# Kernel tuning notes

Hardware: AMD Instinct MI355X
Metric: run time of the kernel (lower is better)

The kernel has to match this reference:

```python
import jax, jax.numpy as jnp
import numpy as np

TEMP = 0.02          # init kwarg temp (sim is multiplied by temp before exp)
OTHERWEIGHT = 0.5    # init kwarg otherweight (cross-half weighting)


def _labels(overlap_inds, bs):
    # labels1: class i for group i of feats1; labels2: same class if overlap,
    # else a fresh class starting at K, incrementing per non-overlap group.
    K = overlap_inds.shape[0]
    labels1 = jnp.repeat(jnp.arange(K), bs)
    non = (overlap_inds == 0).astype(jnp.int32)
    excl = jnp.cumsum(non) - non  # exclusive prefix count of non-overlap groups
    cls2 = jnp.where(overlap_inds.astype(bool), jnp.arange(K), K + excl)
    labels2 = jnp.repeat(cls2, bs)
    return jnp.concatenate([labels1, labels2])


def setup_inputs() -> dict:
    key = jax.random.key(0)
    k1, k2, k3 = jax.random.split(key, 3)
    K, BS, F = 8, 256, 512
    feats1 = jax.random.normal(k1, (K * BS, F), dtype=jnp.float32)
    feats2 = jax.random.normal(k2, (K * BS, F), dtype=jnp.float32)
    overlap_inds = jax.random.randint(k3, (K,), 0, 2).astype(jnp.int32)
    return {"feats1": feats1, "feats2": feats2, "overlap_inds": overlap_inds, "bs": BS}


def reference(feats1, feats2, overlap_inds, bs):
    n1 = feats1.shape[0]
    feats = jnp.concatenate([feats1, feats2])         # [N, F]
    n = feats.shape[0]
    labels = _labels(overlap_inds, bs)                # [N]

    same = labels[None, :] == labels[:, None]         # [N, N] bool
    sim = jnp.exp((feats @ feats.T) * TEMP)           # [N, N]

    eye = jnp.eye(n, dtype=bool)
    pos_mask = same & ~eye
    neg_mask = ~same

    # cross_weighting: OTHERWEIGHT on cross-half blocks, 1.0 within each half
    half = jnp.arange(n) < n1
    cross = jnp.where(half[:, None] == half[None, :], 1.0, OTHERWEIGHT)

    # per-row negative sum; loss = sum over positives of cw * -log(pos/neg_sum)
    neg_sum = jnp.sum(jnp.where(neg_mask, sim, 0.0), axis=1)        # [N]
    loss_terms = jnp.where(pos_mask, cross * -jnp.log(sim / neg_sum[:, None]), 0.0)
    total_pos = jnp.sum(pos_mask).astype(jnp.float32)
    loss = loss_terms.sum() / total_pos

    # accuracy: a positive counts iff it beats every negative in its row
    # (mean(0)==1.0 over strict > comparisons <=> pos > max(neg))
    max_neg = jnp.max(jnp.where(neg_mask, sim, -jnp.inf), axis=1)   # [N]
    correct = jnp.where(pos_mask, (sim > max_neg[:, None]).astype(jnp.float32), 0.0)
    acc = correct.sum() / total_pos
    return acc, loss
```

## Files before the change

kernel.cpp:

```cpp
#include <hip/hip_runtime.h>


#define KGRP 8
#define FD   512
#define N1T  2048
#define NT   4096
#define TEMPW 0.02f

typedef __attribute__((ext_vector_type(8))) short short8;
typedef __attribute__((ext_vector_type(4))) float f32x4;
typedef unsigned short ushort_t;


__device__ __forceinline__ unsigned enc_ord(float f) {
  unsigned u = __float_as_uint(f);
  return (u & 0x80000000u) ? ~u : (u | 0x80000000u);
}
__device__ __forceinline__ float dec_ord(unsigned u) {
  unsigned b = (u & 0x80000000u) ? (u & 0x7fffffffu) : ~u;
  return __uint_as_float(b);
}

__device__ __forceinline__ ushort_t f2bf(float f) {
  unsigned u = __float_as_uint(f);
  u = (u + 0x7fffu + ((u >> 16) & 1u)) >> 16;
  return (ushort_t)u;
}

__device__ __forceinline__ void gld16(const void* g, void* l) {
  __builtin_amdgcn_global_load_lds(
      (const __attribute__((address_space(1))) unsigned*)g,
      (__attribute__((address_space(3))) unsigned*)l, 16, 0, 0);
}

__global__ __launch_bounds__(256) void prep_k(
    const float* __restrict__ f1, const float* __restrict__ f2,
    ushort_t* __restrict__ bf,
    float* __restrict__ neg_sum, unsigned* __restrict__ neg_max,
    float* __restrict__ sumS, float* __restrict__ corr,
    int* __restrict__ cnts, int* __restrict__ neg_list,
    int* __restrict__ pos_list, const int* __restrict__ ov)
{
  const int b = blockIdx.x, t = threadIdx.x;

  {
    int i = b * 256 + t;
    size_t base = (size_t)i * 8;
    const size_t half = (size_t)N1T * FD;
    const float* sp = (base < half) ? (f1 + base) : (f2 + (base - half));
    float4 u0 = ((const float4*)sp)[0];
    float4 u1 = ((const float4*)sp)[1];
    short8 o;
    o[0] = (short)f2bf(u0.x); o[1] = (short)f2bf(u0.y);
    o[2] = (short)f2bf(u0.z); o[3] = (short)f2bf(u0.w);
    o[4] = (short)f2bf(u1.x); o[5] = (short)f2bf(u1.y);
    o[6] = (short)f2bf(u1.z); o[7] = (short)f2bf(u1.w);
    *(short8*)(bf + base) = o;
  }

  if (b >= 1 && b <= 16) {
    int i = (b - 1) * 256 + t;
    neg_sum[i] = 0.f;
    neg_max[i] = 0u;
  }

  if (b == 0) {
    __shared__ int c[16];
    if (t == 0) {
      sumS[0] = 0.f; corr[0] = 0.f; cnts[0] = 0; cnts[1] = 0;
      int excl = 0;
      for (int g = 0; g < KGRP; g++) c[g] = g;
      for (int g = 0; g < KGRP; g++) {
        if (ov[g]) c[KGRP + g] = g;
        else       { c[KGRP + g] = KGRP + excl; excl++; }
      }
    }
    __syncthreads();
    for (int p = t; p < 1024; p += 256) {
      int bi = p >> 5, bj = p & 31;
      if (bj < bi) continue;
      if (c[bi >> 1] == c[bj >> 1]) {
        int k = atomicAdd(&cnts[1], 1); pos_list[k] = (bi << 5) | bj;
      } else {
        int k = atomicAdd(&cnts[0], 1); neg_list[k] = (bi << 5) | bj;
      }
    }
  }
}

__global__ __launch_bounds__(256) void gram_k(
    const ushort_t* __restrict__ bf, const int* __restrict__ cnts,
    const int* __restrict__ neg_list, const int* __restrict__ pos_list,
    float* __restrict__ neg_sum, unsigned* __restrict__ neg_max,
    float* __restrict__ pos_dots)
{
  __shared__ char lds[3 * 16384];

  const int nn = cnts[0];
  const int b  = blockIdx.x;
  const bool isneg = (b < nn);
  const int pr = isneg ? neg_list[b] : pos_list[b - nn];
  const int bi = pr >> 5, bj = pr & 31;
  const int brow = bi << 7, bcol = bj << 7;

  const int t    = threadIdx.x;
  const int lane = t & 63, wave = t >> 6;
  const int wrow = (wave >> 1) << 6, wcol = (wave & 1) << 6;
  const int fr   = lane & 15, fh = lane >> 4;
  const int r_in = t >> 2;
  const int cb   = (t & 3) << 3;
  const int ldsw = wave << 10;

  const ushort_t* gA = bf + (size_t)(brow + r_in) * FD + cb;
  const ushort_t* gB = bf + (size_t)(bcol + r_in) * FD + cb;

  f32x4 acc[4][4];
#pragma unroll
  for (int m = 0; m < 4; m++)
#pragma unroll
    for (int n = 0; n < 4; n++)
      acc[m][n] = (f32x4){0.f, 0.f, 0.f, 0.f};

  auto stage = [&](int buf, int ks) {
    char* dst = lds + buf * 16384 + ldsw;
    const ushort_t* a = gA + (ks << 5);
    const ushort_t* p = gB + (ks << 5);
    gld16(a,                   dst);
    gld16(a + (size_t)64 * FD, dst + 4096);
    gld16(p,                   dst + 8192);
    gld16(p + (size_t)64 * FD, dst + 12288);
  };

  stage(0, 0);
  stage(1, 1);
  int cur = 0;
  for (int kk = 0; kk < 16; kk++) {
    if (kk == 15) asm volatile("s_waitcnt vmcnt(0)" ::: "memory");
    else          asm volatile("s_waitcnt vmcnt(4)" ::: "memory");
    __builtin_amdgcn_s_barrier();
    asm volatile("" ::: "memory");

    char* lA = lds + cur * 16384;
    char* lB = lA + 8192;
    short8 a[4], bb[4];
#pragma unroll
    for (int m = 0; m < 4; m++)
      a[m] = *(const short8*)(lA + ((wrow + (m << 4) + fr) << 6) + (fh << 4));
#pragma unroll
    for (int n = 0; n < 4; n++)
      bb[n] = *(const short8*)(lB + ((wcol + (n << 4) + fr) << 6) + (fh << 4));
#pragma unroll
    for (int m = 0; m < 4; m++)
#pragma unroll
      for (int n = 0; n < 4; n++)
        acc[m][n] = __builtin_amdgcn_mfma_f32_16x16x32_bf16(a[m], bb[n], acc[m][n], 0, 0, 0);

    if (kk + 2 < 16) {
      int nxt = cur - 1; if (nxt < 0) nxt = 2;
      stage(nxt, kk + 2);
    }
    cur = cur + 1; if (cur == 3) cur = 0;
  }

  const int rbase = brow + wrow + (fh << 2);
  const int cbase = bcol + wcol + fr;

  if (isneg) {
    float colS[4] = {0.f, 0.f, 0.f, 0.f};
    float colM[4] = {-3.0e38f, -3.0e38f, -3.0e38f, -3.0e38f};
#pragma unroll
    for (int m = 0; m < 4; m++) {
#pragma unroll
      for (int j = 0; j < 4; j++) {
        float s = 0.f, mx = -3.0e38f;
#pragma unroll
        for (int n = 0; n < 4; n++) {
          float d = acc[m][n][j];
          float e = __expf(d * TEMPW);
          s += e; mx = fmaxf(mx, d);
          colS[n] += e; colM[n] = fmaxf(colM[n], d);
        }
#pragma unroll
        for (int o = 1; o < 16; o <<= 1) {
          s  += __shfl_xor(s, o, 64);
          mx  = fmaxf(mx, __shfl_xor(mx, o, 64));
        }
        if (fr == 0) {
          int r = rbase + (m << 4) + j;
          atomicAdd(&neg_sum[r], s);
          atomicMax(&neg_max[r], enc_ord(mx));
        }
      }
    }
#pragma unroll
    for (int n = 0; n < 4; n++) {
      float s = colS[n], mx = colM[n];
      s += __shfl_xor(s, 16, 64); mx = fmaxf(mx, __shfl_xor(mx, 16, 64));
      s += __shfl_xor(s, 32, 64); mx = fmaxf(mx, __shfl_xor(mx, 32, 64));
      if (fh == 0) {
        int c = cbase + (n << 4);
        atomicAdd(&neg_sum[c], s);
        atomicMax(&neg_max[c], enc_ord(mx));
      }
    }
  } else {
    float* basep = pos_dots + (size_t)(b - nn) * 16384;
#pragma unroll
    for (int m = 0; m < 4; m++)
#pragma unroll
      for (int n = 0; n < 4; n++)
        *(f32x4*)(basep + (((m << 2) + n) << 10) + (t << 2)) = acc[m][n];
  }
}

__global__ __launch_bounds__(256) void pos_cmp_k(
    const float* __restrict__ pos_dots, const int* __restrict__ cnts,
    const int* __restrict__ pos_list, const unsigned* __restrict__ neg_max,
    float* __restrict__ sumS, float* __restrict__ corr)
{
  const int p = blockIdx.x;
  if (p >= cnts[1]) return;
  const int pr = pos_list[p];
  const int bi = pr >> 5, bj = pr & 31;

  const int t = threadIdx.x, lane = t & 63, wave = t >> 6;
  const int wrow = (wave >> 1) << 6, wcol = (wave & 1) << 6;
  const int fr = lane & 15, fh = lane >> 4;
  const int rbase = (bi << 7) + wrow + (fh << 2);
  const int cbase = (bj << 7) + wcol + fr;
  const float cw = ((bi < 16) == (bj < 16)) ? 1.0f : 0.5f;
  const float* basep = pos_dots + (size_t)p * 16384;

  __shared__ float wsum[4];
  __shared__ int   wcnt[4];

  float ssum = 0.f;
  int cc = 0;
  if (bi == bj) {
#pragma unroll
    for (int m = 0; m < 4; m++)
#pragma unroll
      for (int n = 0; n < 4; n++) {
        f32x4 v = *(const f32x4*)(basep + (((m << 2) + n) << 10) + (t << 2));
        int c = cbase + (n << 4);
#pragma unroll
        for (int j = 0; j < 4; j++) {
          int r = rbase + (m << 4) + j;
          if (r != c) {
            float d = v[j];
            ssum += d;
            cc += (d > dec_ord(neg_max[r])) ? 1 : 0;
          }
        }
      }
  } else {
    float nmr[4][4], nmc[4];
#pragma unroll
    for (int m = 0; m < 4; m++)
#pragma unroll
      for (int j = 0; j < 4; j++) nmr[m][j] = dec_ord(neg_max[rbase + (m << 4) + j]);
#pragma unroll
    for (int n = 0; n < 4; n++) nmc[n] = dec_ord(neg_max[cbase + (n << 4)]);
#pragma unroll
    for (int m = 0; m < 4; m++)
#pragma unroll
      for (int n = 0; n < 4; n++) {
        f32x4 v = *(const f32x4*)(basep + (((m << 2) + n) << 10) + (t << 2));
#pragma unroll
        for (int j = 0; j < 4; j++) {
          float d = v[j];
          ssum += d;
          cc += ((d > nmr[m][j]) ? 1 : 0) + ((d > nmc[n]) ? 1 : 0);
        }
      }
    ssum *= 2.0f;
  }
  ssum *= cw;

#pragma unroll
  for (int o = 1; o < 64; o <<= 1) {
    ssum += __shfl_xor(ssum, o, 64);
    cc   += __shfl_xor(cc, o, 64);
  }
  if (lane == 0) { wsum[wave] = ssum; wcnt[wave] = cc; }
  __syncthreads();
  if (t == 0) {
    float S2 = 0.f; int C2 = 0;
    for (int w = 0; w < 4; w++) { S2 += wsum[w]; C2 += wcnt[w]; }
    atomicAdd(sumS, S2);
    atomicAdd(corr, (float)C2);
  }
}

__global__ void fin_k(const float* __restrict__ neg_sum, const float* __restrict__ sumS,
                      const float* __restrict__ corr, const int* __restrict__ ov,
                      float* __restrict__ out)
{
  __shared__ double red[256];
  int t = threadIdx.x;
  double a = 0.0;
  for (int r = t; r < NT; r += 256) {
    int g = r >> 8;
    double W = 255.0 + 128.0 * (ov[g & 7] ? 1.0 : 0.0);
    a += W * log((double)neg_sum[r]);
  }
  red[t] = a;
  __syncthreads();
  if (t == 0) {
    double sw = 0.0;
    for (int i = 0; i < 256; i++) sw += red[i];
    double tp = 0.0;
    for (int g = 0; g < 16; g++) tp += 256.0 * (255.0 + 256.0 * (ov[g & 7] ? 1.0 : 0.0));
    double loss = (sw - (double)TEMPW * (double)sumS[0]) / tp;
    out[0] = (float)((double)corr[0] / tp);
    out[1] = (float)loss;
  }
}


extern "C" void kernel_launch(void* const* d_in, const int* in_sizes, int n_in,
                              void* d_out, int out_size, void* d_ws, size_t ws_size,
                              hipStream_t stream)
{
  const float* f1 = (const float*)d_in[0];
  const float* f2 = (const float*)d_in[1];
  const int*   ov = (const int*)d_in[2];

  char* ws = (char*)d_ws;
  ushort_t* bf       = (ushort_t*)ws;
  float*    neg_sum  = (float*)(ws + (size_t)(4 << 20));
  unsigned* neg_max  = (unsigned*)(ws + (size_t)(4 << 20) + (16 << 10));
  float*    sumS     = (float*)(ws + (size_t)(4 << 20) + (32 << 10));
  float*    corr     = sumS + 1;
  int*      cnts     = (int*)(sumS + 2);
  int*      neg_list = (int*)(ws + (size_t)(4 << 20) + (36 << 10));
  int*      pos_list = (int*)(ws + (size_t)(4 << 20) + (40 << 10));
  float*    pos_dots = (float*)(ws + (size_t)(4 << 20) + (64 << 10));
  float*    out      = (float*)d_out;

  hipLaunchKernelGGL(prep_k, dim3(1024), dim3(256), 0, stream,
                     f1, f2, bf, neg_sum, neg_max, sumS, corr, cnts,
                     neg_list, pos_list, ov);
  hipLaunchKernelGGL(gram_k, dim3(528), dim3(256), 0, stream,
                     bf, cnts, neg_list, pos_list, neg_sum, neg_max, pos_dots);
  hipLaunchKernelGGL(pos_cmp_k, dim3(80), dim3(256), 0, stream,
                     pos_dots, cnts, pos_list, neg_max, sumS, corr);
  hipLaunchKernelGGL(fin_k, dim3(1), dim3(256), 0, stream,
                     neg_sum, sumS, corr, ov, out);
}
```

Measured before the change: 51.72 us.

## Load GEMM operands directly from global and fuse finalize into positive-compare kernel

The gram kernel stops staging bf16 tiles through a triple-buffered LDS pipeline and instead has each lane load its MFMA fragments straight from global memory in a fully unrolled K loop, with occupancy hinted at three blocks per CU. The separate single-block finalize kernel is folded into the positive-compare kernel using a done-counter so the last block computes the loss and accuracy, which removes one launch. The finalize reduction also moves from double to float with fast log. This trades LDS reuse and barrier sync for redundant global/L2 traffic, and lowers the precision of the final sum.

```diff
diff --git a/kernel.cpp b/kernel.cpp
--- a/kernel.cpp
+++ b/kernel.cpp
@@ -25,12 +25,6 @@
   unsigned u = __float_as_uint(f);
   u = (u + 0x7fffu + ((u >> 16) & 1u)) >> 16;
   return (ushort_t)u;
-}
-
-__device__ __forceinline__ void gld16(const void* g, void* l) {
-  __builtin_amdgcn_global_load_lds(
-      (const __attribute__((address_space(1))) unsigned*)g,
-      (__attribute__((address_space(3))) unsigned*)l, 16, 0, 0);
 }
 
 __global__ __launch_bounds__(256) void prep_k(
@@ -67,7 +61,8 @@
   if (b == 0) {
     __shared__ int c[16];
     if (t == 0) {
-      sumS[0] = 0.f; corr[0] = 0.f; cnts[0] = 0; cnts[1] = 0;
+      sumS[0] = 0.f; corr[0] = 0.f;
+      cnts[0] = 0; cnts[1] = 0; cnts[2] = 0;
       int excl = 0;
       for (int g = 0; g < KGRP; g++) c[g] = g;
       for (int g = 0; g < KGRP; g++) {
@@ -88,14 +83,12 @@
   }
 }
 
-__global__ __launch_bounds__(256) void gram_k(
+__global__ __launch_bounds__(256, 3) void gram_k(
     const ushort_t* __restrict__ bf, const int* __restrict__ cnts,
     const int* __restrict__ neg_list, const int* __restrict__ pos_list,
     float* __restrict__ neg_sum, unsigned* __restrict__ neg_max,
     float* __restrict__ pos_dots)
 {
-  __shared__ char lds[3 * 16384];
-
   const int nn = cnts[0];
   const int b  = blockIdx.x;
   const bool isneg = (b < nn);
@@ -107,12 +100,15 @@
   const int lane = t & 63, wave = t >> 6;
   const int wrow = (wave >> 1) << 6, wcol = (wave & 1) << 6;
   const int fr   = lane & 15, fh = lane >> 4;
-  const int r_in = t >> 2;
-  const int cb   = (t & 3) << 3;
-  const int ldsw = wave << 10;
-
-  const ushort_t* gA = bf + (size_t)(brow + r_in) * FD + cb;
-  const ushort_t* gB = bf + (size_t)(bcol + r_in) * FD + cb;
+
+  const ushort_t* pa[4];
+  const ushort_t* pb[4];
+#pragma unroll
+  for (int m = 0; m < 4; m++)
+    pa[m] = bf + (size_t)(brow + wrow + (m << 4) + fr) * FD + (fh << 3);
+#pragma unroll
+  for (int n = 0; n < 4; n++)
+    pb[n] = bf + (size_t)(bcol + wcol + (n << 4) + fr) * FD + (fh << 3);
 
   f32x4 acc[4][4];
 #pragma unroll
@@ -121,45 +117,18 @@
     for (int n = 0; n < 4; n++)
       acc[m][n] = (f32x4){0.f, 0.f, 0.f, 0.f};
 
-  auto stage = [&](int buf, int ks) {
-    char* dst = lds + buf * 16384 + ldsw;
-    const ushort_t* a = gA + (ks << 5);
-    const ushort_t* p = gB + (ks << 5);
-    gld16(a,                   dst);
-    gld16(a + (size_t)64 * FD, dst + 4096);
-    gld16(p,                   dst + 8192);
-    gld16(p + (size_t)64 * FD, dst + 12288);
-  };
-
-  stage(0, 0);
-  stage(1, 1);
-  int cur = 0;
+#pragma unroll
   for (int kk = 0; kk < 16; kk++) {
-    if (kk == 15) asm volatile("s_waitcnt vmcnt(0)" ::: "memory");
-    else          asm volatile("s_waitcnt vmcnt(4)" ::: "memory");
-    __builtin_amdgcn_s_barrier();
-    asm volatile("" ::: "memory");
-
-    char* lA = lds + cur * 16384;
-    char* lB = lA + 8192;
     short8 a[4], bb[4];
 #pragma unroll
-    for (int m = 0; m < 4; m++)
-      a[m] = *(const short8*)(lA + ((wrow + (m << 4) + fr) << 6) + (fh << 4));
-#pragma unroll
-    for (int n = 0; n < 4; n++)
-      bb[n] = *(const short8*)(lB + ((wcol + (n << 4) + fr) << 6) + (fh << 4));
+    for (int m = 0; m < 4; m++) a[m]  = *(const short8*)(pa[m] + (kk << 5));
+#pragma unroll
+    for (int n = 0; n < 4; n++) bb[n] = *(const short8*)(pb[n] + (kk << 5));
 #pragma unroll
     for (int m = 0; m < 4; m++)
 #pragma unroll
       for (int n = 0; n < 4; n++)
         acc[m][n] = __builtin_amdgcn_mfma_f32_16x16x32_bf16(a[m], bb[n], acc[m][n], 0, 0, 0);
-
-    if (kk + 2 < 16) {
-      int nxt = cur - 1; if (nxt < 0) nxt = 2;
-      stage(nxt, kk + 2);
-    }
-    cur = cur + 1; if (cur == 3) cur = 0;
   }
 
   const int rbase = brow + wrow + (fh << 2);
@@ -213,107 +182,116 @@
   }
 }
 
-__global__ __launch_bounds__(256) void pos_cmp_k(
+__global__ __launch_bounds__(256) void pos_fin_k(
     const float* __restrict__ pos_dots, const int* __restrict__ cnts,
     const int* __restrict__ pos_list, const unsigned* __restrict__ neg_max,
-    float* __restrict__ sumS, float* __restrict__ corr)
+    const float* __restrict__ neg_sum, const int* __restrict__ ov,
+    float* __restrict__ sumS, float* __restrict__ corr,
+    int* __restrict__ done, float* __restrict__ out)
 {
-  const int p = blockIdx.x;
-  if (p >= cnts[1]) return;
-  const int pr = pos_list[p];
-  const int bi = pr >> 5, bj = pr & 31;
-
-  const int t = threadIdx.x, lane = t & 63, wave = t >> 6;
-  const int wrow = (wave >> 1) << 6, wcol = (wave & 1) << 6;
-  const int fr = lane & 15, fh = lane >> 4;
-  const int rbase = (bi << 7) + wrow + (fh << 2);
-  const int cbase = (bj << 7) + wcol + fr;
-  const float cw = ((bi < 16) == (bj < 16)) ? 1.0f : 0.5f;
-  const float* basep = pos_dots + (size_t)p * 16384;
+  const int np = cnts[1];
+  const int p  = blockIdx.x;
+  const int t  = threadIdx.x, lane = t & 63, wave = t >> 6;
 
   __shared__ float wsum[4];
   __shared__ int   wcnt[4];
-
-  float ssum = 0.f;
-  int cc = 0;
-  if (bi == bj) {
-#pragma unroll
-    for (int m = 0; m < 4; m++)
-#pragma unroll
-      for (int n = 0; n < 4; n++) {
-        f32x4 v = *(const f32x4*)(basep + (((m << 2) + n) << 10) + (t << 2));
-        int c = cbase + (n << 4);
-#pragma unroll
-        for (int j = 0; j < 4; j++) {
-          int r = rbase + (m << 4) + j;
-          if (r != c) {
+  __shared__ int   amLast;
+
+  if (p < np) {
+    const int pr = pos_list[p];
+    const int bi = pr >> 5, bj = pr & 31;
+    const int wrow = (wave >> 1) << 6, wcol = (wave & 1) << 6;
+    const int fr = lane & 15, fh = lane >> 4;
+    const int rbase = (bi << 7) + wrow + (fh << 2);
+    const int cbase = (bj << 7) + wcol + fr;
+    const float cw = ((bi < 16) == (bj < 16)) ? 1.0f : 0.5f;
+    const float* basep = pos_dots + (size_t)p * 16384;
+
+    float ssum = 0.f;
+    int cc = 0;
+    if (bi == bj) {
+#pragma unroll
+      for (int m = 0; m < 4; m++)
+#pragma unroll
+        for (int n = 0; n < 4; n++) {
+          f32x4 v = *(const f32x4*)(basep + (((m << 2) + n) << 10) + (t << 2));
+          int c = cbase + (n << 4);
+#pragma unroll
+          for (int j = 0; j < 4; j++) {
+            int r = rbase + (m << 4) + j;
+            if (r != c) {
+              float d = v[j];
+              ssum += d;
+              cc += (d > dec_ord(neg_max[r])) ? 1 : 0;
+            }
+          }
+        }
+    } else {
+      float nmr[4][4], nmc[4];
+#pragma unroll
+      for (int m = 0; m < 4; m++)
+#pragma unroll
+        for (int j = 0; j < 4; j++) nmr[m][j] = dec_ord(neg_max[rbase + (m << 4) + j]);
+#pragma unroll
+      for (int n = 0; n < 4; n++) nmc[n] = dec_ord(neg_max[cbase + (n << 4)]);
+#pragma unroll
+      for (int m = 0; m < 4; m++)
+#pragma unroll
+        for (int n = 0; n < 4; n++) {
+          f32x4 v = *(const f32x4*)(basep + (((m << 2) + n) << 10) + (t << 2));
+#pragma unroll
+          for (int j = 0; j < 4; j++) {
             float d = v[j];
             ssum += d;
-            cc += (d > dec_ord(neg_max[r])) ? 1 : 0;
+            cc += ((d > nmr[m][j]) ? 1 : 0) + ((d > nmc[n]) ? 1 : 0);
           }
         }
-      }
-  } else {
-    float nmr[4][4], nmc[4];
-#pragma unroll
-    for (int m = 0; m < 4; m++)
-#pragma unroll
-      for (int j = 0; j < 4; j++) nmr[m][j] = dec_ord(neg_max[rbase + (m << 4) + j]);
-#pragma unroll
-    for (int n = 0; n < 4; n++) nmc[n] = dec_ord(neg_max[cbase + (n << 4)]);
-#pragma unroll
-    for (int m = 0; m < 4; m++)
-#pragma unroll
-      for (int n = 0; n < 4; n++) {
-        f32x4 v = *(const f32x4*)(basep + (((m << 2) + n) << 10) + (t << 2));
-#pragma unroll
-        for (int j = 0; j < 4; j++) {
-          float d = v[j];
-          ssum += d;
-          cc += ((d > nmr[m][j]) ? 1 : 0) + ((d > nmc[n]) ? 1 : 0);
-        }
-      }
-    ssum *= 2.0f;
-  }
-  ssum *= cw;
-
-#pragma unroll
-  for (int o = 1; o < 64; o <<= 1) {
-    ssum += __shfl_xor(ssum, o, 64);
-    cc   += __shfl_xor(cc, o, 64);
-  }
-  if (lane == 0) { wsum[wave] = ssum; wcnt[wave] = cc; }
+      ssum *= 2.0f;
+    }
+    ssum *= cw;
+
+#pragma unroll
+    for (int o = 1; o < 64; o <<= 1) {
+      ssum += __shfl_xor(ssum, o, 64);
+      cc   += __shfl_xor(cc, o, 64);
+    }
+    if (lane == 0) { wsum[wave] = ssum; wcnt[wave] = cc; }
+    __syncthreads();
+    if (t == 0) {
+      float S2 = 0.f; int C2 = 0;
+      for (int w = 0; w < 4; w++) { S2 += wsum[w]; C2 += wcnt[w]; }
+      atomicAdd(sumS, S2);
+      atomicAdd(corr, (float)C2);
+    }
+  }
+
+  if (t == 0) {
+    int my = -1;
+    if (p < np) { __threadfence(); my = atomicAdd(done, 1); }
+    amLast = (my == np - 1) ? 1 : 0;
+  }
+  __syncthreads();
+  if (!amLast) return;
+  __threadfence();
+
+  float aa = 0.f;
+  for (int r = t; r < NT; r += 256) {
+    int g = r >> 8;
+    float W = ov[g & 7] ? 383.f : 255.f;
+    aa += W * __logf(neg_sum[r]);
+  }
+#pragma unroll
+  for (int o = 1; o < 64; o <<= 1) aa += __shfl_xor(aa, o, 64);
+  if (lane == 0) wsum[wave] = aa;
   __syncthreads();
   if (t == 0) {
-    float S2 = 0.f; int C2 = 0;
-    for (int w = 0; w < 4; w++) { S2 += wsum[w]; C2 += wcnt[w]; }
-    atomicAdd(sumS, S2);
-    atomicAdd(corr, (float)C2);
-  }
-}
-
-__global__ void fin_k(const float* __restrict__ neg_sum, const float* __restrict__ sumS,
-                      const float* __restrict__ corr, const int* __restrict__ ov,
-                      float* __restrict__ out)
-{
-  __shared__ double red[256];
-  int t = threadIdx.x;
-  double a = 0.0;
-  for (int r = t; r < NT; r += 256) {
-    int g = r >> 8;
-    double W = 255.0 + 128.0 * (ov[g & 7] ? 1.0 : 0.0);
-    a += W * log((double)neg_sum[r]);
-  }
-  red[t] = a;
-  __syncthreads();
-  if (t == 0) {
-    double sw = 0.0;
-    for (int i = 0; i < 256; i++) sw += red[i];
-    double tp = 0.0;
-    for (int g = 0; g < 16; g++) tp += 256.0 * (255.0 + 256.0 * (ov[g & 7] ? 1.0 : 0.0));
-    double loss = (sw - (double)TEMPW * (double)sumS[0]) / tp;
-    out[0] = (float)((double)corr[0] / tp);
-    out[1] = (float)loss;
+    float sw = wsum[0] + wsum[1] + wsum[2] + wsum[3];
+    float S = atomicAdd(sumS, 0.f);
+    float C = atomicAdd(corr, 0.f);
+    float tp = 0.f;
+    for (int g = 0; g < 16; g++) tp += 256.f * (255.f + 256.f * (ov[g & 7] ? 1.f : 0.f));
+    out[0] = C / tp;
+    out[1] = (sw - TEMPW * S) / tp;
   }
 }
 
@@ -333,6 +311,7 @@
   float*    sumS     = (float*)(ws + (size_t)(4 << 20) + (32 << 10));
   float*    corr     = sumS + 1;
   int*      cnts     = (int*)(sumS + 2);
+  int*      done     = cnts + 2;
   int*      neg_list = (int*)(ws + (size_t)(4 << 20) + (36 << 10));
   int*      pos_list = (int*)(ws + (size_t)(4 << 20) + (40 << 10));
   float*    pos_dots = (float*)(ws + (size_t)(4 << 20) + (64 << 10));
@@ -343,8 +322,7 @@
                      neg_list, pos_list, ov);
   hipLaunchKernelGGL(gram_k, dim3(528), dim3(256), 0, stream,
                      bf, cnts, neg_list, pos_list, neg_sum, neg_max, pos_dots);
-  hipLaunchKernelGGL(pos_cmp_k, dim3(80), dim3(256), 0, stream,
-                     pos_dots, cnts, pos_list, neg_max, sumS, corr);
-  hipLaunchKernelGGL(fin_k, dim3(1), dim3(256), 0, stream,
-                     neg_sum, sumS, corr, ov, out);
-}
+  hipLaunchKernelGGL(pos_fin_k, dim3(80), dim3(256), 0, stream,
+                     pos_dots, cnts, pos_list, neg_max, neg_sum, ov,
+                     sumS, corr, done, out);
+}
```

Measured after the change: 76.39 us. +47.7%, slower.
